# Kernel optimization log

Hardware: AMD Instinct MI355X
Metric: run time of the kernel (lower is better)

## Reference

```python
import jax, jax.numpy as jnp
import numpy as np

N_TOKEN = 267735
CUTOFFS = [20000, 40000, 200000, 267735]
ENDS = [0] + CUTOFFS
CLUSTER_DIMS = [1024, 256, 64, 16]   # d_embed // div_val**i
CLUSTER_SIZES = [20000, 20000, 160000, 67735]
D_PROJ = 1024
T, B = 256, 4
N_CLUSTERS = 3


def setup_inputs() -> dict:
    key = jax.random.key(0)
    ks = jax.random.split(key, 16)
    inp = {}
    inp["hidden"] = jax.random.normal(ks[0], (T, B, D_PROJ), jnp.float32)
    inp["target"] = jax.random.randint(ks[1], (T, B), 0, N_TOKEN)
    for i in range(4):
        inp[f"W{i}"] = jax.random.normal(ks[2 + 3 * i], (CLUSTER_SIZES[i], CLUSTER_DIMS[i]), jnp.float32) * 0.02
        inp[f"b{i}"] = jnp.zeros((CLUSTER_SIZES[i],), jnp.float32)
        inp[f"P{i}"] = jax.random.normal(ks[3 + 3 * i], (CLUSTER_DIMS[i], D_PROJ), jnp.float32) * 0.02
    inp["cluster_weight"] = jax.random.normal(ks[14], (N_CLUSTERS, 1024), jnp.float32) * 0.02
    inp["cluster_bias"] = jnp.zeros((N_CLUSTERS,), jnp.float32)
    return inp


def _logit(x, W, b, P):
    # x: [T,B,d_proj], P: [e,d_proj], W: [n,e] -> [T,B,n]
    y = jnp.einsum('ibd,ed->ibe', x, P)
    return jnp.einsum('ibe,ne->ibn', y, W) + b


def _gather(logprob, tgt):
    # pick logprob[t, b, tgt[t,b]]
    return jnp.take_along_axis(logprob, tgt[..., None], axis=-1)[..., 0]


def reference(hidden, target, W0, b0, P0, W1, b1, P1, W2, b2, P2, W3, b3, P3,
              cluster_weight, cluster_bias):
    Ws = [W0, W1, W2, W3]
    bs = [b0, b1, b2, b3]
    Ps = [P0, P1, P2, P3]
    loss = jnp.zeros(target.shape, jnp.float32)
    head_logprob = None
    for i in range(4):
        l_idx, r_idx = ENDS[i], ENDS[i + 1]
        mask = (target >= l_idx) & (target < r_idx)
        cur_t = jnp.maximum(jnp.minimum(target, r_idx - 1) - l_idx, 0)
        if i == 0:
            Wh = jnp.concatenate([W0, cluster_weight], axis=0)
            bh = jnp.concatenate([b0, cluster_bias], axis=0)
            head_logprob = jax.nn.log_softmax(_logit(hidden, Wh, bh, P0), axis=-1)
            cur_loss = _gather(head_logprob, cur_t)
        else:
            tail_logprob = jax.nn.log_softmax(_logit(hidden, Ws[i], bs[i], Ps[i]), axis=-1)
            logprob_i = head_logprob[..., CUTOFFS[0] + i - 1, None] + tail_logprob
            cur_loss = _gather(logprob_i, cur_t)
        loss = jnp.where(mask, cur_loss, loss)
    return jnp.mean(-loss)
```

## Files before the change

kernel.cpp:

```cpp
#include <hip/hip_runtime.h>
#include <math.h>

typedef short short8 __attribute__((ext_vector_type(8)));
typedef float f32x4 __attribute__((ext_vector_type(4)));
typedef unsigned long long u64;

#define LOG2E 1.4426950408889634f

__device__ __forceinline__ unsigned short f2bf_rne(float f) {
    unsigned u = __float_as_uint(f);
    unsigned r = (u + 0x7fff + ((u >> 16) & 1)) >> 16;
    return (unsigned short)r;
}
__device__ __forceinline__ float bf2f(unsigned short h) {
    return __uint_as_float(((unsigned)h) << 16);
}
__device__ __forceinline__ void load_lds16(const void* g, void* l) {
    __builtin_amdgcn_global_load_lds((const __attribute__((address_space(1))) void*)g,
                                     (__attribute__((address_space(3))) void*)l,
                                     16, 0, 0);
}
__device__ __forceinline__ u64 pack8_fp8(const float* v, float s) {
    int lo = 0, hi = 0;
    lo = __builtin_amdgcn_cvt_pk_fp8_f32(v[0] * s, v[1] * s, lo, false);
    lo = __builtin_amdgcn_cvt_pk_fp8_f32(v[2] * s, v[3] * s, lo, true);
    hi = __builtin_amdgcn_cvt_pk_fp8_f32(v[4] * s, v[5] * s, hi, false);
    hi = __builtin_amdgcn_cvt_pk_fp8_f32(v[6] * s, v[7] * s, hi, true);
    return (u64)(unsigned)lo | ((u64)(unsigned)hi << 32);
}

__global__ void cvt_h(const float* __restrict__ in, unsigned short* __restrict__ out)
{
    const int i = blockIdx.x * 256 + threadIdx.x;
    const float4 v = *(const float4*)(in + (size_t)i * 4);
    ushort4 h;
    h.x = f2bf_rne(v.x); h.y = f2bf_rne(v.y);
    h.z = f2bf_rne(v.z); h.w = f2bf_rne(v.w);
    *(ushort4*)(out + (size_t)i * 4) = h;
}

struct ProjDesc {
    const float* B;
    unsigned short* Cbf;
    unsigned char* Cf8;
    int ldc; int nreal; int N; int Kpad; int gy_begin;
};

__global__ __launch_bounds__(256) void prepproj(
    const unsigned short* __restrict__ A,
    ProjDesc p0, ProjDesc p1, ProjDesc p2, ProjDesc p3,
    const float* __restrict__ W0, const float* __restrict__ cw,
    const float* __restrict__ W1, const float* __restrict__ W2,
    const float* __restrict__ W3,
    const float* __restrict__ b0, const float* __restrict__ cb,
    const float* __restrict__ b1, const float* __restrict__ b2,
    const float* __restrict__ b3,
    unsigned char* __restrict__ Wb0, unsigned char* __restrict__ Wb1,
    unsigned char* __restrict__ Wb2, unsigned char* __restrict__ Wb3,
    float* __restrict__ bp)
{
    __shared__ char smem[34816];

    const int tid = threadIdx.x;
    const int bx = blockIdx.x;

    if (bx >= 96) {
        const unsigned E0 = 1286144u;
        const unsigned E1 = 1613824u;
        const unsigned E2 = 2260992u;
        const unsigned E3 = 2539520u;
        const unsigned E4 = 2607520u;
        const unsigned stride = (gridDim.x - 96) * 256u;
        for (unsigned u = (bx - 96) * 256u + tid; u < E4; u += stride) {
            if (u < E3) {
                const float* src = nullptr;
                unsigned char* dstm; unsigned tile, kg2, r, tstride;
                if (u < E0) {
                    tile = u >> 13; const unsigned rem = u & 8191u;
                    kg2 = rem >> 7; r = rem & 127u;
                    const unsigned row = tile * 128u + r;
                    if (row < 20000u)      src = W0 + (size_t)row * 1024 + kg2 * 16;
                    else if (row < 20003u) src = cw + (size_t)(row - 20000u) * 1024 + kg2 * 16;
                    dstm = Wb0; tstride = 131072u;
                } else if (u < E1) {
                    const unsigned j = u - E0;
                    tile = j >> 11; const unsigned rem = j & 2047u;
                    kg2 = rem >> 7; r = rem & 127u;
                    const unsigned row = tile * 128u + r;
                    if (row < 20000u) src = W1 + (size_t)row * 256 + kg2 * 16;
                    dstm = Wb1; tstride = 32768u;
                } else if (u < E2) {
                    const unsigned j = u - E1;
                    tile = j >> 9; kg2 = (j >> 7) & 3u; r = j & 127u;
                    const unsigned row = tile * 128u + r;
                    if (row < 160000u) src = W2 + (size_t)row * 64 + kg2 * 16;
                    dstm = Wb2; tstride = 8192u;
                } else {
                    const unsigned j = u - E2;
                    tile = j >> 9; kg2 = (j >> 7) & 3u; r = j & 127u;
                    const unsigned row = tile * 128u + r;
                    if (kg2 == 0 && row < 67735u) src = W3 + (size_t)row * 16;
                    dstm = Wb3; tstride = 8192u;
                }
                float f[16];
                if (src) {
#pragma unroll
                    for (int q = 0; q < 4; ++q) {
                        const float4 v = *(const float4*)(src + q * 4);
                        f[q * 4 + 0] = v.x; f[q * 4 + 1] = v.y;
                        f[q * 4 + 2] = v.z; f[q * 4 + 3] = v.w;
                    }
                } else {
#pragma unroll
                    for (int q = 0; q < 16; ++q) f[q] = 0.f;
                }
                u64* dst = (u64*)(dstm + (size_t)tile * tstride);
                dst[(2 * kg2) * 128 + r]     = pack8_fp8(f,     16.0f);
                dst[(2 * kg2 + 1) * 128 + r] = pack8_fp8(f + 8, 16.0f);
            } else {
                const unsigned idx0 = (u - E3) * 4u;
                float e[4];
#pragma unroll
                for (int j = 0; j < 4; ++j) {
                    const unsigned idx = idx0 + j;
                    float v;
                    if (idx < 20096u) {
                        v = (idx < 20000u) ? b0[idx] * LOG2E
                          : (idx < 20003u) ? cb[idx - 20000u] * LOG2E : -1e30f;
                    } else if (idx < 40576u) {
                        const unsigned i1 = idx - 20096u;
                        v = (i1 < 20000u) ? b1[i1] * LOG2E : -1e30f;
                    } else if (idx < 202368u) {
                        const unsigned i2 = idx - 40576u;
                        v = (i2 < 160000u) ? b2[i2] * LOG2E : -1e30f;
                    } else {
                        const unsigned i3 = idx - 202368u;
                        v = (i3 < 67735u) ? b3[i3] * LOG2E : -1e30f;
                    }
                    e[j] = v;
                }
                *(float4*)(bp + idx0) = make_float4(e[0], e[1], e[2], e[3]);
            }
        }
        return;
    }

    unsigned short* As = (unsigned short*)smem;
    unsigned short* Bs = (unsigned short*)(smem + 16384);

    const int mt = bx & 7;
    const int py = bx >> 3;
    ProjDesc p = (py >= p3.gy_begin) ? p3 : (py >= p2.gy_begin) ? p2
               : (py >= p1.gy_begin) ? p1 : p0;

    const int w = tid >> 6;
    const int l = tid & 63;
    const int m0 = mt * 128;
    const int n0 = (py - p.gy_begin) * 128;
    const int wm = (w >> 1) * 64;
    const int wn = (w & 1) * 64;
    const int lane16 = l & 15;
    const int quad = l >> 4;

    const unsigned short* aptr[4];
    int ag_base[4];
#pragma unroll
    for (int i = 0; i < 4; ++i) {
        const int g = w * 256 + i * 64 + l;
        aptr[i] = A + (size_t)(m0 + (g & 127)) * 1024 + (g >> 7) * 8;
        ag_base[i] = (w * 256 + i * 64) * 8;
    }

    const int bn = tid >> 1;
    const int bhalf = tid & 1;
    int brow = n0 + bn;
    if (brow > p.N - 1) brow = p.N - 1;
    const float* brow_ptr = p.B + (size_t)brow * 1024;

    f32x4 acc[4][4] = {};

    for (int k0 = 0; k0 < 1024; k0 += 64) {
        __syncthreads();
#pragma unroll
        for (int i = 0; i < 4; ++i)
            load_lds16(aptr[i] + k0, (void*)&As[ag_base[i]]);
#pragma unroll
        for (int j = 0; j < 8; ++j) {
            const int kq = bhalf * 8 + j;
            const float4 v = *(const float4*)(brow_ptr + k0 + kq * 4);
            const unsigned px = __builtin_amdgcn_perm(__float_as_uint(v.y), __float_as_uint(v.x), 0x07060302);
            const unsigned pyv = __builtin_amdgcn_perm(__float_as_uint(v.w), __float_as_uint(v.z), 0x07060302);
            const int gran = (kq >> 1) * 128 + bn;
            *(uint2*)&Bs[gran * 8 + (kq & 1) * 4] = make_uint2(px, pyv);
        }
        __syncthreads();

#pragma unroll
        for (int kk = 0; kk < 2; ++kk) {
            const int kgb = kk * 4 + quad;
            short8 af[4], bfr[4];
#pragma unroll
            for (int mi = 0; mi < 4; ++mi)
                af[mi] = *(const short8*)&As[(kgb * 128 + wm + mi * 16 + lane16) * 8];
#pragma unroll
            for (int ni = 0; ni < 4; ++ni)
                bfr[ni] = *(const short8*)&Bs[(kgb * 128 + wn + ni * 16 + lane16) * 8];
#pragma unroll
            for (int mi = 0; mi < 4; ++mi)
#pragma unroll
                for (int ni = 0; ni < 4; ++ni)
                    acc[mi][ni] = __builtin_amdgcn_mfma_f32_16x16x32_bf16(
                        af[mi], bfr[ni], acc[mi][ni], 0, 0, 0);
        }
    }

#pragma unroll
    for (int mi = 0; mi < 4; ++mi)
#pragma unroll
        for (int ni = 0; ni < 4; ++ni) {
            const int n = n0 + wn + ni * 16 + lane16;
            if (n < p.ldc) {
#pragma unroll
                for (int r = 0; r < 4; ++r) {
                    const int m = m0 + wm + mi * 16 + quad * 4 + r;
                    const float v = (n < p.nreal) ? acc[mi][ni][r] : 0.f;
                    p.Cbf[(size_t)m * p.ldc + n] = f2bf_rne(v);
                }
            }
        }

    float* bounce = (float*)smem;
    u64* Yout = (u64*)p.Cf8 + (size_t)mt * 16 * p.Kpad;
    for (int c = 0; c < 2; ++c) {
        const int colbase = n0 + c * 64;
        if (colbase >= p.Kpad) break;
        __syncthreads();
        if ((w & 1) == c) {
#pragma unroll
            for (int mi = 0; mi < 4; ++mi)
#pragma unroll
                for (int ni = 0; ni < 4; ++ni) {
                    const int ncol = ni * 16 + lane16;
                    const bool real = (colbase + ncol) < p.nreal;
#pragma unroll
                    for (int r = 0; r < 4; ++r) {
                        const int m = wm + mi * 16 + quad * 4 + r;
                        bounce[m * 66 + ncol] = real ? acc[mi][ni][r] : 0.f;
                    }
                }
        }
        __syncthreads();
#pragma unroll
        for (int i = 0; i < 4; ++i) {
            const int g = i * 256 + tid;
            const int kgl = g >> 7;
            const int m = g & 127;
            float v[8];
#pragma unroll
            for (int j = 0; j < 8; ++j) v[j] = bounce[m * 66 + kgl * 8 + j];
            Yout[((colbase >> 3) + kgl) * 128 + m] = pack8_fp8(v, 4.0f);
        }
    }
}

struct ExpDesc {
    const unsigned char* A;
    const unsigned char* W;
    const float* bias;
    float* part;
    int Kpad; int ksl; int kmask; int gy_begin; int slab;
};

__global__ __launch_bounds__(256) void exp_gemm(ExpDesc d0, ExpDesc d1, ExpDesc d2, ExpDesc d3)
{
    __shared__ u64 As[2][1024];
    __shared__ u64 Bs[2][1024];
    __shared__ float buf[128][2];

    const int gy = blockIdx.y;
    ExpDesc d = (gy >= d3.gy_begin) ? d3 : (gy >= d2.gy_begin) ? d2
              : (gy >= d1.gy_begin) ? d1 : d0;

    const int tid = threadIdx.x;
    const int w = tid >> 6;
    const int l = tid & 63;
    const int mt = blockIdx.x;
    const int wm = (w >> 1) * 64;
    const int wn = (w & 1) * 64;
    const int lane16 = l & 15;
    const int quad = l >> 4;

    const int tiles_begin = (gy - d.gy_begin) * d.slab;
    const int T = d.slab << d.ksl;
    const int kmask = d.kmask;
    const int ksl = d.ksl;

    const size_t tstride = (size_t)128 * d.Kpad;
    const unsigned char* Abase = d.A + (size_t)mt * tstride;
    const unsigned char* Bbase = d.W + (size_t)tiles_begin * tstride;

    const int so0 = tid * 16;
    const int so1 = 4096 + tid * 16;

    load_lds16(Abase + so0, (char*)As[0] + so0);
    load_lds16(Abase + so1, (char*)As[0] + so1);
    load_lds16(Bbase + so0, (char*)Bs[0] + so0);
    load_lds16(Bbase + so1, (char*)Bs[0] + so1);

    float biasc[4], biasn[4];
#pragma unroll
    for (int ni = 0; ni < 4; ++ni)
        biasc[ni] = d.bias[tiles_begin * 128 + wn + ni * 16 + lane16];
#pragma unroll
    for (int ni = 0; ni < 4; ++ni) biasn[ni] = 0.f;

    f32x4 acc[4][4] = {};
    float rowsum[4][4] = {};
    const float c1 = LOG2E / 64.0f;

    for (int it = 0; it < T; ++it) {
        const int slot = it & 1;
        __syncthreads();

        if (it + 1 < T) {
            const int ns = slot ^ 1;
            const int kc = (it + 1) & kmask;
            if (kmask) {
                const unsigned char* ac = Abase + kc * 8192;
                load_lds16(ac + so0, (char*)As[ns] + so0);
                load_lds16(ac + so1, (char*)As[ns] + so1);
            }
            const unsigned char* bc = Bbase + (size_t)((it + 1) >> ksl) * tstride + kc * 8192;
            load_lds16(bc + so0, (char*)Bs[ns] + so0);
            load_lds16(bc + so1, (char*)Bs[ns] + so1);
            if (kc == 0) {
#pragma unroll
                for (int ni = 0; ni < 4; ++ni)
                    biasn[ni] = d.bias[(tiles_begin + ((it + 1) >> ksl)) * 128 + wn + ni * 16 + lane16];
            }
        }

        const u64* Ar = As[kmask ? slot : 0];
        const u64* Br = Bs[slot];
#pragma unroll
        for (int ks = 0; ks < 2; ++ks) {
            u64 af[4], bfr[4];
#pragma unroll
            for (int mi = 0; mi < 4; ++mi)
                af[mi] = Ar[(ks * 4 + quad) * 128 + wm + mi * 16 + lane16];
#pragma unroll
            for (int ni = 0; ni < 4; ++ni)
                bfr[ni] = Br[(ks * 4 + quad) * 128 + wn + ni * 16 + lane16];
#pragma unroll
            for (int mi = 0; mi < 4; ++mi)
#pragma unroll
                for (int ni = 0; ni < 4; ++ni)
                    acc[mi][ni] = __builtin_amdgcn_mfma_f32_16x16x32_fp8_fp8(
                        (long)af[mi], (long)bfr[ni], acc[mi][ni], 0, 0, 0);
        }

        if ((it & kmask) == kmask) {
#pragma unroll
            for (int mi = 0; mi < 4; ++mi)
#pragma unroll
                for (int r = 0; r < 4; ++r) {
                    float s = exp2f(fmaf(acc[mi][0][r], c1, biasc[0]))
                            + exp2f(fmaf(acc[mi][1][r], c1, biasc[1]))
                            + exp2f(fmaf(acc[mi][2][r], c1, biasc[2]))
                            + exp2f(fmaf(acc[mi][3][r], c1, biasc[3]));
                    rowsum[mi][r] += s;
                }
#pragma unroll
            for (int mi = 0; mi < 4; ++mi)
#pragma unroll
                for (int ni = 0; ni < 4; ++ni)
                    acc[mi][ni] = (f32x4){0.f, 0.f, 0.f, 0.f};
#pragma unroll
            for (int ni = 0; ni < 4; ++ni) biasc[ni] = biasn[ni];
        }
    }

#pragma unroll
    for (int off = 1; off < 16; off <<= 1)
#pragma unroll
        for (int mi = 0; mi < 4; ++mi)
#pragma unroll
            for (int r = 0; r < 4; ++r)
                rowsum[mi][r] += __shfl_xor(rowsum[mi][r], off, 64);

    __syncthreads();
    if (lane16 == 0) {
#pragma unroll
        for (int mi = 0; mi < 4; ++mi)
#pragma unroll
            for (int r = 0; r < 4; ++r)
                buf[wm + mi * 16 + quad * 4 + r][wn >> 6] = rowsum[mi][r];
    }
    __syncthreads();
    if (tid < 128)
        d.part[(size_t)(gy - d.gy_begin) * 1024 + mt * 128 + tid] = buf[tid][0] + buf[tid][1];
}

__global__ void redext(const float* __restrict__ p0, const float* __restrict__ p1,
                       const float* __restrict__ p2, const float* __restrict__ p3,
                       float* __restrict__ S,
                       const unsigned short* __restrict__ Y0, const unsigned short* __restrict__ Y1,
                       const unsigned short* __restrict__ Y2, const unsigned short* __restrict__ Y3,
                       const int* __restrict__ target,
                       const float* __restrict__ W0, const float* __restrict__ b0,
                       const float* __restrict__ W1, const float* __restrict__ b1,
                       const float* __restrict__ W2, const float* __restrict__ b2,
                       const float* __restrict__ W3, const float* __restrict__ b3,
                       const float* __restrict__ cw, const float* __restrict__ cb,
                       float* __restrict__ headlogit, float* __restrict__ taillogit)
{
    if (blockIdx.x < 16) {
        const int idx = blockIdx.x * 256 + threadIdx.x;
        const int c = idx >> 10, m = idx & 1023;
        const float* p = (c == 0) ? p0 : (c == 1) ? p1 : (c == 2) ? p2 : p3;
        const int G = (c == 0) ? 157 : (c == 1) ? 40 : (c == 2) ? 79 : 34;
        float s = 0.f;
        for (int y = 0; y < G; ++y) s += p[(size_t)y * 1024 + m];
        S[idx] = s;
        return;
    }
    const int token = (blockIdx.x - 16) * 4 + (threadIdx.x >> 6);
    const int lane = threadIdx.x & 63;
    const int tgt = target[token];
    const int ci = (tgt < 20000) ? 0 : (tgt < 40000) ? 1 : (tgt < 200000) ? 2 : 3;

    {
        const int h = (ci == 0) ? tgt : (20000 + ci - 1);
        const float* row;
        float bb;
        if (h < 20000) { row = W0 + (size_t)h * 1024; bb = b0[h]; }
        else           { row = cw + (size_t)(h - 20000) * 1024; bb = cb[h - 20000]; }
        const unsigned short* y = Y0 + (size_t)token * 1024;
        float s = 0.f;
        for (int k = lane; k < 1024; k += 64) s += bf2f(y[k]) * row[k];
#pragma unroll
        for (int off = 1; off < 64; off <<= 1) s += __shfl_xor(s, off, 64);
        if (lane == 0) headlogit[token] = s + bb;
    }

    float tl = 0.f;
    if (ci > 0) {
        const unsigned short* Y; const float* W; const float* b; int K, ldy, lidx;
        if (ci == 1)      { Y = Y1; W = W1; b = b1; K = 256; ldy = 256; lidx = 20000; }
        else if (ci == 2) { Y = Y2; W = W2; b = b2; K = 64;  ldy = 64;  lidx = 40000; }
        else              { Y = Y3; W = W3; b = b3; K = 16;  ldy = 64;  lidx = 200000; }
        const int r = tgt - lidx;
        const unsigned short* y = Y + (size_t)token * ldy;
        const float* row = W + (size_t)r * K;
        float s = 0.f;
        for (int k = lane; k < K; k += 64) s += bf2f(y[k]) * row[k];
#pragma unroll
        for (int off = 1; off < 64; off <<= 1) s += __shfl_xor(s, off, 64);
        tl = s + b[r];
    }
    if (lane == 0) taillogit[token] = tl;
}

__global__ void finalize_kernel(const float* __restrict__ S,
                                const int* __restrict__ target,
                                const float* __restrict__ headlogit,
                                const float* __restrict__ taillogit,
                                float* __restrict__ out)
{
    __shared__ float red[256];
    const int tid = threadIdx.x;
    float acc = 0.f;
    for (int token = tid; token < 1024; token += 256) {
        const int tgt = target[token];
        const int ci = (tgt < 20000) ? 0 : (tgt < 40000) ? 1 : (tgt < 200000) ? 2 : 3;
        float lp = headlogit[token] - logf(S[token]);
        if (ci > 0)
            lp += taillogit[token] - logf(S[ci * 1024 + token]);
        acc -= lp;
    }
    red[tid] = acc;
    __syncthreads();
    for (int s = 128; s > 0; s >>= 1) {
        if (tid < s) red[tid] += red[tid + s];
        __syncthreads();
    }
    if (tid == 0) out[0] = red[0] * (1.0f / 1024.0f);
}

extern "C" void kernel_launch(void* const* d_in, const int* in_sizes, int n_in,
                              void* d_out, int out_size, void* d_ws, size_t ws_size,
                              hipStream_t stream)
{
    const float* hidden = (const float*)d_in[0];
    const int*   target = (const int*)d_in[1];
    const float* W0 = (const float*)d_in[2];  const float* b0 = (const float*)d_in[3];  const float* P0 = (const float*)d_in[4];
    const float* W1 = (const float*)d_in[5];  const float* b1 = (const float*)d_in[6];  const float* P1 = (const float*)d_in[7];
    const float* W2 = (const float*)d_in[8];  const float* b2 = (const float*)d_in[9];  const float* P2 = (const float*)d_in[10];
    const float* W3 = (const float*)d_in[11]; const float* b3 = (const float*)d_in[12]; const float* P3 = (const float*)d_in[13];
    const float* cw = (const float*)d_in[14]; const float* cb = (const float*)d_in[15];
    float* out = (float*)d_out;

    unsigned char* ws = (unsigned char*)d_ws;
    unsigned short* h_bf = (unsigned short*)ws;
    unsigned short* Y0bf = (unsigned short*)(ws + 2097152);
    unsigned short* Y1bf = (unsigned short*)(ws + 4194304);
    unsigned short* Y2bf = (unsigned short*)(ws + 4718592);
    unsigned short* Y3bf = (unsigned short*)(ws + 4849664);
    unsigned char* Y0f8 = ws + 4980736;
    unsigned char* Y1f8 = ws + 6029312;
    unsigned char* Y2f8 = ws + 6291456;
    unsigned char* Y3f8 = ws + 6356992;
    unsigned char* Wb0 = ws + 6422528;
    unsigned char* Wb1 = ws + 27000832;
    unsigned char* Wb2 = ws + 32243712;
    unsigned char* Wb3 = ws + 42598400;
    float* bp = (float*)(ws + 47054848);

    float* part0 = (float*)ws;
    float* part1 = part0 + (size_t)157 * 1024;
    float* part2 = part1 + (size_t)40 * 1024;
    float* part3 = part2 + (size_t)79 * 1024;
    float* S = part3 + (size_t)34 * 1024;
    float* headlogit = S + 4096;
    float* taillogit = headlogit + 1024;

    cvt_h<<<1024, 256, 0, stream>>>(hidden, h_bf);

    ProjDesc pr0 = { P0, Y0bf, Y0f8, 1024, 1024, 1024, 1024, 0 };
    ProjDesc pr1 = { P1, Y1bf, Y1f8, 256,  256,  256,  256,  8 };
    ProjDesc pr2 = { P2, Y2bf, Y2f8, 64,   64,   64,   64,   10 };
    ProjDesc pr3 = { P3, Y3bf, Y3f8, 64,   16,   16,   64,   11 };
    prepproj<<<2048, 256, 0, stream>>>(h_bf, pr0, pr1, pr2, pr3,
                                       W0, cw, W1, W2, W3,
                                       b0, cb, b1, b2, b3,
                                       Wb0, Wb1, Wb2, Wb3, bp);

    ExpDesc d0 = { Y0f8, Wb0, bp,          part0, 1024, 4, 15, 0,   1 };
    ExpDesc d1 = { Y1f8, Wb1, bp + 20096,  part1, 256,  2, 3,  157, 4 };
    ExpDesc d2 = { Y2f8, Wb2, bp + 40576,  part2, 64,   0, 0,  197, 16 };
    ExpDesc d3 = { Y3f8, Wb3, bp + 202368, part3, 64,   0, 0,  276, 16 };
    exp_gemm<<<dim3(8, 310), 256, 0, stream>>>(d0, d1, d2, d3);

    redext<<<272, 256, 0, stream>>>(part0, part1, part2, part3, S,
                                    Y0bf, Y1bf, Y2bf, Y3bf, target,
                                    W0, b0, W1, b1, W2, b2, W3, b3,
                                    cw, cb, headlogit, taillogit);

    finalize_kernel<<<1, 256, 0, stream>>>(S, target, headlogit, taillogit, out);
}
```

Baseline: 436.2 us.

## Pipeline exp_gemm loads two stages ahead, stage bias in LDS, remap blocks

Restructures the exp_gemm main loop so that global-to-LDS loads are issued two iterations ahead. Explicit vmcnt waits and raw barriers replace the single __syncthreads per iteration. The bias for the whole slab is preloaded into LDS once, removing per-tile global bias loads from the loop. The 2D grid becomes a 1D grid with a remapping of block index to (mt, gy) so that blocks sharing a W slab are spread across XCDs/CUs differently. The changes add hand-tuned wait counts that depend on how many loads each thread issues, which makes correctness fragile, and a second barrier per iteration.

```diff
diff --git a/kernel.cpp b/kernel.cpp
--- a/kernel.cpp
+++ b/kernel.cpp
@@ -19,6 +19,10 @@
     __builtin_amdgcn_global_load_lds((const __attribute__((address_space(1))) void*)g,
                                      (__attribute__((address_space(3))) void*)l,
                                      16, 0, 0);
+}
+template<int N>
+__device__ __forceinline__ void waitvm() {
+    asm volatile("s_waitcnt vmcnt(%0)" :: "n"(N) : "memory");
 }
 __device__ __forceinline__ u64 pack8_fp8(const float* v, float s) {
     int lo = 0, hi = 0;
@@ -275,16 +279,20 @@
 {
     __shared__ u64 As[2][1024];
     __shared__ u64 Bs[2][1024];
+    __shared__ float biasLds[2048];
     __shared__ float buf[128][2];
 
-    const int gy = blockIdx.y;
+    const int wg = blockIdx.x;
+    const int orig = (wg & 7) * 310 + (wg >> 3);
+    const int mt = orig & 7;
+    const int gy = orig >> 3;
+
     ExpDesc d = (gy >= d3.gy_begin) ? d3 : (gy >= d2.gy_begin) ? d2
               : (gy >= d1.gy_begin) ? d1 : d0;
 
     const int tid = threadIdx.x;
     const int w = tid >> 6;
     const int l = tid & 63;
-    const int mt = blockIdx.x;
     const int wm = (w >> 1) * 64;
     const int wn = (w & 1) * 64;
     const int lane16 = l & 15;
@@ -294,6 +302,7 @@
     const int T = d.slab << d.ksl;
     const int kmask = d.kmask;
     const int ksl = d.ksl;
+    const bool haveA = (kmask != 0);
 
     const size_t tstride = (size_t)128 * d.Kpad;
     const unsigned char* Abase = d.A + (size_t)mt * tstride;
@@ -302,17 +311,27 @@
     const int so0 = tid * 16;
     const int so1 = 4096 + tid * 16;
 
+    {
+        const float* bsrc = d.bias + (size_t)tiles_begin * 128;
+        const int nb = d.slab * 32;
+        for (int u = tid; u < nb; u += 256)
+            load_lds16(bsrc + u * 4, (char*)biasLds + u * 16);
+    }
     load_lds16(Abase + so0, (char*)As[0] + so0);
     load_lds16(Abase + so1, (char*)As[0] + so1);
     load_lds16(Bbase + so0, (char*)Bs[0] + so0);
     load_lds16(Bbase + so1, (char*)Bs[0] + so1);
-
-    float biasc[4], biasn[4];
-#pragma unroll
-    for (int ni = 0; ni < 4; ++ni)
-        biasc[ni] = d.bias[tiles_begin * 128 + wn + ni * 16 + lane16];
-#pragma unroll
-    for (int ni = 0; ni < 4; ++ni) biasn[ni] = 0.f;
+    {
+        const int kc = 1 & kmask;
+        if (haveA) {
+            const unsigned char* ac = Abase + kc * 8192;
+            load_lds16(ac + so0, (char*)As[1] + so0);
+            load_lds16(ac + so1, (char*)As[1] + so1);
+        }
+        const unsigned char* bc = Bbase + (size_t)(1 >> ksl) * tstride + kc * 8192;
+        load_lds16(bc + so0, (char*)Bs[1] + so0);
+        load_lds16(bc + so1, (char*)Bs[1] + so1);
+    }
 
     f32x4 acc[4][4] = {};
     float rowsum[4][4] = {};
@@ -320,27 +339,12 @@
 
     for (int it = 0; it < T; ++it) {
         const int slot = it & 1;
-        __syncthreads();
-
-        if (it + 1 < T) {
-            const int ns = slot ^ 1;
-            const int kc = (it + 1) & kmask;
-            if (kmask) {
-                const unsigned char* ac = Abase + kc * 8192;
-                load_lds16(ac + so0, (char*)As[ns] + so0);
-                load_lds16(ac + so1, (char*)As[ns] + so1);
-            }
-            const unsigned char* bc = Bbase + (size_t)((it + 1) >> ksl) * tstride + kc * 8192;
-            load_lds16(bc + so0, (char*)Bs[ns] + so0);
-            load_lds16(bc + so1, (char*)Bs[ns] + so1);
-            if (kc == 0) {
-#pragma unroll
-                for (int ni = 0; ni < 4; ++ni)
-                    biasn[ni] = d.bias[(tiles_begin + ((it + 1) >> ksl)) * 128 + wn + ni * 16 + lane16];
-            }
-        }
-
-        const u64* Ar = As[kmask ? slot : 0];
+        if (it + 1 < T) { if (haveA) waitvm<4>(); else waitvm<2>(); }
+        else            { waitvm<0>(); }
+        __builtin_amdgcn_s_barrier();
+        __builtin_amdgcn_sched_barrier(0);
+
+        const u64* Ar = haveA ? As[slot] : As[0];
         const u64* Br = Bs[slot];
 #pragma unroll
         for (int ks = 0; ks < 2; ++ks) {
@@ -360,6 +364,11 @@
         }
 
         if ((it & kmask) == kmask) {
+            const int tile = it >> ksl;
+            float biasc[4];
+#pragma unroll
+            for (int ni = 0; ni < 4; ++ni)
+                biasc[ni] = biasLds[tile * 128 + wn + ni * 16 + lane16];
 #pragma unroll
             for (int mi = 0; mi < 4; ++mi)
 #pragma unroll
@@ -375,8 +384,22 @@
 #pragma unroll
                 for (int ni = 0; ni < 4; ++ni)
                     acc[mi][ni] = (f32x4){0.f, 0.f, 0.f, 0.f};
-#pragma unroll
-            for (int ni = 0; ni < 4; ++ni) biasc[ni] = biasn[ni];
+        }
+
+        __builtin_amdgcn_sched_barrier(0);
+        __builtin_amdgcn_s_barrier();
+
+        if (it + 2 < T) {
+            const int nit = it + 2;
+            const int kc = nit & kmask;
+            if (haveA) {
+                const unsigned char* ac = Abase + kc * 8192;
+                load_lds16(ac + so0, (char*)As[slot] + so0);
+                load_lds16(ac + so1, (char*)As[slot] + so1);
+            }
+            const unsigned char* bc = Bbase + (size_t)(nit >> ksl) * tstride + kc * 8192;
+            load_lds16(bc + so0, (char*)Bs[slot] + so0);
+            load_lds16(bc + so1, (char*)Bs[slot] + so1);
         }
     }
 
@@ -539,7 +562,7 @@
     ExpDesc d1 = { Y1f8, Wb1, bp + 20096,  part1, 256,  2, 3,  157, 4 };
     ExpDesc d2 = { Y2f8, Wb2, bp + 40576,  part2, 64,   0, 0,  197, 16 };
     ExpDesc d3 = { Y3f8, Wb3, bp + 202368, part3, 64,   0, 0,  276, 16 };
-    exp_gemm<<<dim3(8, 310), 256, 0, stream>>>(d0, d1, d2, d3);
+    exp_gemm<<<2480, 256, 0, stream>>>(d0, d1, d2, d3);
 
     redext<<<272, 256, 0, stream>>>(part0, part1, part2, part3, S,
                                     Y0bf, Y1bf, Y2bf, Y3bf, target,
```

Result: slower. 501.5 us (+15.0%).
